# Kernel optimization log

Hardware: AMD Instinct MI355X
Metric: run time of the kernel (lower is better)

## Reference

```python
import jax, jax.numpy as jnp
import numpy as np
from jax.ops import segment_sum, segment_max

DIM = 32   # hidden dim (hardcoded in Net)
N = 10000  # nodes
E = 160000 # edges
B = 64     # graphs in batch


def setup_inputs():
    key = jax.random.key(0)
    ks = jax.random.split(key, 16)
    r = lambda k, s: jax.random.normal(k, s, dtype=jnp.float32) * 0.1
    z = lambda s: jnp.zeros(s, jnp.float32)
    return {
        "x": jax.random.normal(ks[0], (N, 1), jnp.float32),
        "edge_attr": jax.random.normal(ks[1], (E, 2), jnp.float32),
        "lin0_w": r(ks[2], (1, DIM)), "lin0_b": z((DIM,)),
        "nn_w1": r(ks[3], (2, 128)), "nn_b1": z((128,)),
        "nn_w2": r(ks[4], (128, DIM * DIM)), "nn_b2": z((DIM * DIM,)),
        "conv_root": r(ks[5], (DIM, DIM)), "conv_bias": z((DIM,)),
        "gru_w_ih": r(ks[6], (DIM, 3 * DIM)), "gru_w_hh": r(ks[7], (DIM, 3 * DIM)),
        "gru_b_ih": z((3 * DIM,)), "gru_b_hh": z((3 * DIM,)),
        "lstm_w_ih": r(ks[8], (2 * DIM, 4 * DIM)), "lstm_w_hh": r(ks[9], (DIM, 4 * DIM)),
        "lstm_b_ih": z((4 * DIM,)), "lstm_b_hh": z((4 * DIM,)),
        "lin1_w": r(ks[10], (2 * DIM, DIM)), "lin1_b": z((DIM,)),
        "lin2_w": r(ks[11], (DIM, 1)), "lin2_b": z((1,)),
        "edge_index": jax.random.randint(ks[12], (2, E), 0, N),
        "batch": jnp.sort(jax.random.randint(ks[13], (N,), 0, B)),
    }


def _forward(x, edge_attr, params, edge_index, batch):
    (lin0_w, lin0_b, nn_w1, nn_b1, nn_w2, nn_b2, conv_root, conv_bias,
     gru_w_ih, gru_w_hh, gru_b_ih, gru_b_hh,
     lstm_w_ih, lstm_w_hh, lstm_b_ih, lstm_b_hh,
     lin1_w, lin1_b, lin2_w, lin2_b) = params
    src, dst = edge_index[0], edge_index[1]
    deg = jnp.maximum(segment_sum(jnp.ones((E,), x.dtype), dst, num_segments=N), 1.0)[:, None]
    # edge-conditioned weight matrices (depend only on edge_attr -> compute once)
    ew = (jax.nn.relu(edge_attr @ nn_w1 + nn_b1) @ nn_w2 + nn_b2).reshape(E, DIM, DIM)

    out = jax.nn.relu(x @ lin0_w + lin0_b)  # (N, DIM)
    h = out                                  # GRU hidden state
    for _ in range(3):
        # NNConv: gather -> per-edge matmul -> scatter-mean, plus root weight + bias
        msg = jnp.einsum('ei,eio->eo', out[src], ew)          # (E, DIM)
        agg = segment_sum(msg, dst, num_segments=N) / deg      # (N, DIM)
        m = jax.nn.relu(agg + out @ conv_root + conv_bias)
        # single GRU step (seq_len = 1)
        gi = m @ gru_w_ih + gru_b_ih
        gh = h @ gru_w_hh + gru_b_hh
        i_r, i_z, i_n = jnp.split(gi, 3, axis=-1)
        h_r, h_z, h_n = jnp.split(gh, 3, axis=-1)
        rg = jax.nn.sigmoid(i_r + h_r)
        zg = jax.nn.sigmoid(i_z + h_z)
        ng = jnp.tanh(i_n + rg * h_n)
        h = (1.0 - zg) * ng + zg * h
        out = h

    # Set2Set pooling, 3 processing steps
    q_star = jnp.zeros((B, 2 * DIM), x.dtype)
    hh = jnp.zeros((B, DIM), x.dtype)
    cc = jnp.zeros((B, DIM), x.dtype)
    for _ in range(3):
        gates = q_star @ lstm_w_ih + lstm_b_ih + hh @ lstm_w_hh + lstm_b_hh
        ig, fg, gg, og = jnp.split(gates, 4, axis=-1)  # torch gate order i,f,g,o
        cc = jax.nn.sigmoid(fg) * cc + jax.nn.sigmoid(ig) * jnp.tanh(gg)
        hh = jax.nn.sigmoid(og) * jnp.tanh(cc)
        q = hh                                          # (B, DIM)
        e = jnp.sum(out * q[batch], axis=-1)            # (N,)
        a = jnp.exp(e - segment_max(e, batch, num_segments=B)[batch])
        a = a / segment_sum(a, batch, num_segments=B)[batch]
        rvec = segment_sum(a[:, None] * out, batch, num_segments=B)  # (B, DIM)
        q_star = jnp.concatenate([q, rvec], axis=-1)

    y = jax.nn.relu(q_star @ lin1_w + lin1_b)
    return (y @ lin2_w + lin2_b).reshape(-1)  # (B,)


def reference(x, edge_attr, lin0_w, lin0_b, nn_w1, nn_b1, nn_w2, nn_b2, conv_root, conv_bias, gru_w_ih, gru_w_hh, gru_b_ih, gru_b_hh, lstm_w_ih, lstm_w_hh, lstm_b_ih, lstm_b_hh, lin1_w, lin1_b, lin2_w, lin2_b, edge_index, batch):
    params = (lin0_w, lin0_b, nn_w1, nn_b1, nn_w2, nn_b2, conv_root, conv_bias,
              gru_w_ih, gru_w_hh, gru_b_ih, gru_b_hh,
              lstm_w_ih, lstm_w_hh, lstm_b_ih, lstm_b_hh,
              lin1_w, lin1_b, lin2_w, lin2_b)
    return _forward(x, edge_attr, params, edge_index, batch)
```

## Files before the change

kernel.cpp:

```cpp
#include <hip/hip_runtime.h>
#include <math.h>

#define NN 10000
#define NE 160000
#define NG 64
#define DIM 32
#define CAP 96

typedef __attribute__((ext_vector_type(8))) short bf16x8;
typedef __attribute__((ext_vector_type(4))) float f32x4;

__device__ __forceinline__ float sigmoidf_(float x) { return 1.f / (1.f + expf(-x)); }

__device__ __forceinline__ unsigned short f2bf(float x) {
    unsigned u = __float_as_uint(x);
    u += 0x7FFF + ((u >> 16) & 1);
    return (unsigned short)(u >> 16);
}
__device__ __forceinline__ float bf2f(unsigned short b) {
    return __uint_as_float(((unsigned)b) << 16);
}

__global__ void k_setup(const float* __restrict__ w2, unsigned short* __restrict__ w2f,
                        const float* __restrict__ x, const float* __restrict__ lw,
                        const float* __restrict__ lb, float* __restrict__ out,
                        const int* __restrict__ batch, int* __restrict__ gstart,
                        const int* __restrict__ ei, const float* __restrict__ ea,
                        int* __restrict__ cursor,
                        int* __restrict__ srt_src, float* __restrict__ srt_ea) {
    int b = blockIdx.x, t = threadIdx.x;
    if (b < 512) {
        int tid = b * 256 + t;
        int h = tid >> 10, rem = tid & 1023, i = rem >> 5, n = rem & 31;
        float v = w2[tid];
        unsigned short hi = f2bf(v);
        unsigned short lo = f2bf(v - bf2f(hi));
        int s = h >> 5, hm = h & 31, q = hm >> 3, j = hm & 7;
        int tile = n >> 4, nn = n & 15, lane = q * 16 + nn;
        int c = (i * 4 + s) * 2 + tile;
        w2f[(c * 2 + 0) * 512 + lane * 8 + j] = hi;
        w2f[(c * 2 + 1) * 512 + lane * 8 + j] = lo;
    } else if (b < 1762) {
        int idx = (b - 512) * 256 + t;
        int n = idx >> 5, d = idx & 31;
        out[idx] = fmaxf(x[n] * lw[d] + lb[d], 0.f);
    } else if (b == 1762) {
        if (t <= NG) {
            int g = t, lo = 0, hi = NN;
            while (lo < hi) { int mid = (lo + hi) >> 1; if (batch[mid] < g) lo = mid + 1; else hi = mid; }
            gstart[g] = lo;
        }
    } else {
        int e = (b - 1763) * 256 + t;
        if (e < NE) {
            int d = ei[NE + e];
            int p = atomicAdd(&cursor[d], 1);
            int pos = d * CAP + p;
            srt_src[pos] = ei[e];
            srt_ea[2 * pos]     = ea[2 * e];
            srt_ea[2 * pos + 1] = ea[2 * e + 1];
        }
    }
}

#define NS 1040
#define PS 8320
__global__ __launch_bounds__(512, 4) void k_conv_gru(
    const int* __restrict__ cursor, const int* __restrict__ srt_src,
    const float* __restrict__ srt_ea,
    const float* __restrict__ w1, const float* __restrict__ b1,
    const unsigned short* __restrict__ w2f, const float* __restrict__ b2,
    const float* __restrict__ out_old,
    float* __restrict__ Sg,
    const float* __restrict__ root, const float* __restrict__ cbias,
    const float* __restrict__ wih, const float* __restrict__ whh,
    const float* __restrict__ bih, const float* __restrict__ bhh,
    float* __restrict__ out_new)
{
    __shared__ __align__(16) unsigned short RB[2 * PS];
    int t = threadIdx.x;
    int wave = t >> 6, lane = t & 63;
    int n0 = blockIdx.x * 8;
    int n = n0 + wave;

    float Racc[64];
    #pragma unroll
    for (int i = 0; i < 64; ++i) Racc[i] = 0.f;
    float sacc = 0.f;

    float w1a0 = w1[lane],      w1c0 = w1[128 + lane],  bb0 = b1[lane];
    float w1a1 = w1[64 + lane], w1c1 = w1[192 + lane],  bb1 = b1[64 + lane];

    int rs = n * CAP;
    int re = rs + cursor[n];
    const float2* eap = (const float2*)srt_ea;

    int p = rs;
    for (; p + 1 < re; p += 2) {
        int s0 = __builtin_amdgcn_readfirstlane(srt_src[p]);
        int s1 = __builtin_amdgcn_readfirstlane(srt_src[p + 1]);
        float2 a0 = eap[p];
        float2 a1 = eap[p + 1];
        const float* o0 = out_old + s0 * DIM;
        const float* o1 = out_old + s1 * DIM;
        float r00 = fmaxf(a0.x * w1a0 + a0.y * w1c0 + bb0, 0.f);
        float r01 = fmaxf(a0.x * w1a1 + a0.y * w1c1 + bb1, 0.f);
        float r10 = fmaxf(a1.x * w1a0 + a1.y * w1c0 + bb0, 0.f);
        float r11 = fmaxf(a1.x * w1a1 + a1.y * w1c1 + bb1, 0.f);
        #pragma unroll
        for (int q = 0; q < 32; ++q) {
            float v0 = o0[q];
            Racc[q]      += r00 * v0;
            Racc[32 + q] += r01 * v0;
        }
        #pragma unroll
        for (int q = 0; q < 32; ++q) {
            float v1 = o1[q];
            Racc[q]      += r10 * v1;
            Racc[32 + q] += r11 * v1;
        }
        if (lane < DIM) sacc += o0[lane] + o1[lane];
    }
    if (p < re) {
        int s0 = __builtin_amdgcn_readfirstlane(srt_src[p]);
        float2 a0 = eap[p];
        const float* o0 = out_old + s0 * DIM;
        float r00 = fmaxf(a0.x * w1a0 + a0.y * w1c0 + bb0, 0.f);
        float r01 = fmaxf(a0.x * w1a1 + a0.y * w1c1 + bb1, 0.f);
        #pragma unroll
        for (int q = 0; q < 32; ++q) {
            float v0 = o0[q];
            Racc[q]      += r00 * v0;
            Racc[32 + q] += r01 * v0;
        }
        if (lane < DIM) sacc += o0[lane];
    }
    if (lane < DIM) Sg[n * DIM + lane] = sacc;

    int quad = lane >> 4;
    int mm = lane & 7;
    unsigned aoff = (unsigned)(mm * NS + wave * 128 + quad * 8);
    f32x4 acc0 = {0.f, 0.f, 0.f, 0.f};
    f32x4 acc1 = {0.f, 0.f, 0.f, 0.f};

    unsigned short* Hw = RB + wave * NS;
    unsigned short* Lw = RB + PS + wave * NS;

    #pragma unroll
    for (int pass = 0; pass < 4; ++pass) {
        if (pass) __syncthreads();
        #pragma unroll
        for (int li = 0; li < 8; ++li) {
            float v0 = Racc[pass * 8 + li];
            float v1 = Racc[32 + pass * 8 + li];
            unsigned short h0 = f2bf(v0);
            unsigned short l0 = f2bf(v0 - bf2f(h0));
            unsigned short h1 = f2bf(v1);
            unsigned short l1 = f2bf(v1 - bf2f(h1));
            Hw[li * 128 + lane] = h0;  Hw[li * 128 + 64 + lane] = h1;
            Lw[li * 128 + lane] = l0;  Lw[li * 128 + 64 + lane] = l1;
        }
        __syncthreads();
        int ig = pass * 8 + wave;
        #pragma unroll
        for (int s = 0; s < 4; ++s) {
            bf16x8 ah = *(const bf16x8*)(RB + aoff + s * 32);
            bf16x8 al = *(const bf16x8*)(RB + PS + aoff + s * 32);
            const unsigned short* bp = w2f + (unsigned)((ig * 4 + s) * 2048 + lane * 8);
            bf16x8 bh0 = *(const bf16x8*)(bp);
            bf16x8 bl0 = *(const bf16x8*)(bp + 512);
            bf16x8 bh1 = *(const bf16x8*)(bp + 1024);
            bf16x8 bl1 = *(const bf16x8*)(bp + 1536);
            acc0 = __builtin_amdgcn_mfma_f32_16x16x32_bf16(ah, bh0, acc0, 0, 0, 0);
            acc0 = __builtin_amdgcn_mfma_f32_16x16x32_bf16(ah, bl0, acc0, 0, 0, 0);
            acc0 = __builtin_amdgcn_mfma_f32_16x16x32_bf16(al, bh0, acc0, 0, 0, 0);
            acc1 = __builtin_amdgcn_mfma_f32_16x16x32_bf16(ah, bh1, acc1, 0, 0, 0);
            acc1 = __builtin_amdgcn_mfma_f32_16x16x32_bf16(ah, bl1, acc1, 0, 0, 0);
            acc1 = __builtin_amdgcn_mfma_f32_16x16x32_bf16(al, bh1, acc1, 0, 0, 0);
        }
    }
    __syncthreads();

    float* part = (float*)RB;
    #pragma unroll
    for (int r = 0; r < 4; ++r) {
        part[((wave * 2 + 0) * 64 + lane) * 4 + r] = acc0[r];
        part[((wave * 2 + 1) * 64 + lane) * 4 + r] = acc1[r];
    }
    __syncthreads();

    if (t < 256) {
        int nb = t >> 5, d = t & 31;
        int nn_ = n0 + nb;
        int base = t & 32;
        int tile = d >> 4, col = d & 15;
        int lidx = (nb >> 2) * 16 + col, reg = nb & 3;
        float aggv = 0.f;
        #pragma unroll
        for (int wv = 0; wv < 8; ++wv)
            aggv += part[((wv * 2 + tile) * 64 + lidx) * 4 + reg];

        float bt = 0.f;
        #pragma unroll 8
        for (int i = 0; i < DIM; ++i) bt += Sg[nn_ * DIM + i] * b2[i * DIM + d];
        int cdeg = cursor[nn_];
        float degf = (float)(cdeg > 0 ? cdeg : 1);
        aggv = (aggv + bt) / degf;

        float x = out_old[nn_ * DIM + d];
        float rootsum = 0.f;
        #pragma unroll 8
        for (int k = 0; k < DIM; ++k)
            rootsum += __shfl(x, base + k) * root[k * DIM + d];
        float m = fmaxf(aggv + rootsum + cbias[d], 0.f);

        float gir = bih[d], giz = bih[DIM + d], gin = bih[2 * DIM + d];
        float ghr = bhh[d], ghz = bhh[DIM + d], ghn = bhh[2 * DIM + d];
        #pragma unroll 4
        for (int k = 0; k < DIM; ++k) {
            float mk = __shfl(m, base + k);
            float hk = __shfl(x, base + k);
            gir += mk * wih[k * 96 + d];
            giz += mk * wih[k * 96 + DIM + d];
            gin += mk * wih[k * 96 + 2 * DIM + d];
            ghr += hk * whh[k * 96 + d];
            ghz += hk * whh[k * 96 + DIM + d];
            ghn += hk * whh[k * 96 + 2 * DIM + d];
        }
        float rg = sigmoidf_(gir + ghr);
        float zg = sigmoidf_(giz + ghz);
        float ng = tanhf(gin + rg * ghn);
        out_new[nn_ * DIM + d] = (1.f - zg) * ng + zg * x;
    }
}

__global__ __launch_bounds__(256) void k_set2set(
    const float* __restrict__ out, const int* __restrict__ gstart,
    const float* __restrict__ wih, const float* __restrict__ whh,
    const float* __restrict__ bih, const float* __restrict__ bhh,
    const float* __restrict__ l1w, const float* __restrict__ l1b,
    const float* __restrict__ l2w, const float* __restrict__ l2b,
    float* __restrict__ ebuf, float* __restrict__ y)
{
    __shared__ float swih[64 * 128];
    __shared__ float swhh[32 * 128];
    __shared__ float sq[2 * DIM];
    __shared__ float shh[DIM], scc[DIM];
    __shared__ float sgates[4 * DIM];
    __shared__ float sacc[8][DIM];
    __shared__ float sredA[4], sredB[4];

    int g = blockIdx.x, t = threadIdx.x;
    {
        const float4* wv = (const float4*)wih;   float4* sv = (float4*)swih;
        for (int i = t; i < 2048; i += 256) sv[i] = wv[i];
        const float4* wv2 = (const float4*)whh;  float4* sv2 = (float4*)swhh;
        for (int i = t; i < 1024; i += 256) sv2[i] = wv2[i];
    }
    if (t < 2 * DIM) sq[t] = 0.f;
    if (t < DIM) { shh[t] = 0.f; scc[t] = 0.f; }
    int ns = gstart[g], ne = gstart[g + 1];
    __syncthreads();

    for (int step = 0; step < 3; ++step) {
        if (t < 128) {
            float acc = bih[t] + bhh[t];
            #pragma unroll 8
            for (int k = 0; k < 2 * DIM; ++k) acc += sq[k] * swih[k * 128 + t];
            #pragma unroll 8
            for (int k = 0; k < DIM; ++k)     acc += shh[k] * swhh[k * 128 + t];
            sgates[t] = acc;
        }
        __syncthreads();
        if (t < DIM) {
            float ig = sigmoidf_(sgates[t]);
            float fg = sigmoidf_(sgates[DIM + t]);
            float gg = tanhf(sgates[2 * DIM + t]);
            float og = sigmoidf_(sgates[3 * DIM + t]);
            float c_new = fg * scc[t] + ig * gg;
            float h_new = og * tanhf(c_new);
            scc[t] = c_new;
            shh[t] = h_new;
            sq[t] = h_new;
        }
        __syncthreads();

        float lmax = -3.0e38f;
        for (int n = ns + t; n < ne; n += 256) {
            const float4* orow = (const float4*)(out + n * DIM);
            float e = 0.f;
            #pragma unroll
            for (int q = 0; q < 8; ++q) {
                float4 o4 = orow[q];
                e += o4.x * shh[4 * q] + o4.y * shh[4 * q + 1]
                   + o4.z * shh[4 * q + 2] + o4.w * shh[4 * q + 3];
            }
            ebuf[n] = e;
            lmax = fmaxf(lmax, e);
        }
        #pragma unroll
        for (int s = 1; s < 64; s <<= 1) lmax = fmaxf(lmax, __shfl_xor(lmax, s));
        if ((t & 63) == 0) sredA[t >> 6] = lmax;
        __syncthreads();
        float M = fmaxf(fmaxf(sredA[0], sredA[1]), fmaxf(sredA[2], sredA[3]));

        float lsum = 0.f;
        for (int n = ns + t; n < ne; n += 256) {
            float v = expf(ebuf[n] - M);
            ebuf[n] = v;
            lsum += v;
        }
        #pragma unroll
        for (int s = 1; s < 64; s <<= 1) lsum += __shfl_xor(lsum, s);
        if ((t & 63) == 0) sredB[t >> 6] = lsum;
        __syncthreads();
        float S = sredB[0] + sredB[1] + sredB[2] + sredB[3];
        float inv = (S > 0.f) ? 1.f / S : 0.f;

        int stp = t >> 5, d = t & 31;
        float racc = 0.f;
        for (int n = ns + stp; n < ne; n += 8)
            racc += ebuf[n] * out[n * DIM + d];
        sacc[stp][d] = racc;
        __syncthreads();
        if (t < DIM) {
            float r = 0.f;
            #pragma unroll
            for (int s = 0; s < 8; ++s) r += sacc[s][t];
            sq[DIM + t] = r * inv;
        }
        __syncthreads();
    }

    if (t < DIM) {
        float h = l1b[t];
        #pragma unroll 8
        for (int k = 0; k < 2 * DIM; ++k) h += sq[k] * l1w[k * DIM + t];
        float v = fmaxf(h, 0.f) * l2w[t];
        #pragma unroll
        for (int s = 1; s < 32; s <<= 1) v += __shfl_xor(v, s);
        if (t == 0) y[g] = v + l2b[0];
    }
}

extern "C" void kernel_launch(void* const* d_in, const int* in_sizes, int n_in,
                              void* d_out, int out_size, void* d_ws, size_t ws_size,
                              hipStream_t stream) {
    const float* x         = (const float*)d_in[0];
    const float* edge_attr = (const float*)d_in[1];
    const float* lin0_w    = (const float*)d_in[2];
    const float* lin0_b    = (const float*)d_in[3];
    const float* nn_w1     = (const float*)d_in[4];
    const float* nn_b1     = (const float*)d_in[5];
    const float* nn_w2     = (const float*)d_in[6];
    const float* nn_b2     = (const float*)d_in[7];
    const float* conv_root = (const float*)d_in[8];
    const float* conv_bias = (const float*)d_in[9];
    const float* gru_w_ih  = (const float*)d_in[10];
    const float* gru_w_hh  = (const float*)d_in[11];
    const float* gru_b_ih  = (const float*)d_in[12];
    const float* gru_b_hh  = (const float*)d_in[13];
    const float* lstm_w_ih = (const float*)d_in[14];
    const float* lstm_w_hh = (const float*)d_in[15];
    const float* lstm_b_ih = (const float*)d_in[16];
    const float* lstm_b_hh = (const float*)d_in[17];
    const float* lin1_w    = (const float*)d_in[18];
    const float* lin1_b    = (const float*)d_in[19];
    const float* lin2_w    = (const float*)d_in[20];
    const float* lin2_b    = (const float*)d_in[21];
    const int*   edge_index= (const int*)d_in[22];
    const int*   batch     = (const int*)d_in[23];
    float* yout = (float*)d_out;

    char* p = (char*)d_ws;
    auto alloc = [&](size_t bytes) { char* r = p; p += (bytes + 255) & ~(size_t)255; return r; };

    int*   cursor = (int*)  alloc(NN * sizeof(int));
    size_t zero_bytes = (size_t)(p - (char*)d_ws);
    int*   gstart    = (int*)  alloc((NG + 1) * sizeof(int));
    int*   srt_src   = (int*)  alloc((size_t)NN * CAP * sizeof(int));
    float* srt_ea    = (float*)alloc((size_t)NN * CAP * 2 * sizeof(float));
    float* outA      = (float*)alloc(NN * DIM * sizeof(float));
    float* outB      = (float*)alloc(NN * DIM * sizeof(float));
    float* Sg        = (float*)alloc(NN * DIM * sizeof(float));
    unsigned short* w2f = (unsigned short*)alloc(262144 * sizeof(unsigned short));
    float* ebuf      = (float*)alloc(NN * sizeof(float));
    (void)ws_size; (void)n_in; (void)in_sizes; (void)out_size;

    hipMemsetAsync(d_ws, 0, zero_bytes, stream);

    k_setup<<<2388, 256, 0, stream>>>(nn_w2, w2f, x, lin0_w, lin0_b, outA, batch, gstart,
                                      edge_index, edge_attr, cursor, srt_src, srt_ea);

    const float* cur = outA;
    float* nxt = outB;
    for (int it = 0; it < 3; ++it) {
        k_conv_gru<<<1250, 512, 0, stream>>>(cursor, srt_src, srt_ea,
                                             nn_w1, nn_b1, w2f, nn_b2,
                                             cur, Sg,
                                             conv_root, conv_bias,
                                             gru_w_ih, gru_w_hh, gru_b_ih, gru_b_hh,
                                             nxt);
        const float* tmp = nxt; nxt = (float*)cur; cur = tmp;
    }
    const float* outF = cur;

    k_set2set<<<NG, 256, 0, stream>>>(outF, gstart,
                                      lstm_w_ih, lstm_w_hh, lstm_b_ih, lstm_b_hh,
                                      lin1_w, lin1_b, lin2_w, lin2_b, ebuf, yout);
}
```

Baseline: 327.8 us.

## Sort nodes by degree for balanced blocks and preload edge lists per wave

Adds a single-block k_perm kernel that buckets nodes by in-degree (descending) into a permutation, so each 8-wave conv block handles nodes of similar degree and waves inside a block wait less on each other. The conv kernel also loads up to 64 edge sources and attributes per wave in one coalesced load and broadcasts them with readlane, replacing per-edge scalar loads. The per-node neighbor sum moves from a global Sg buffer into shared memory, using all 64 lanes before a final shuffle reduction. It adds an extra serial kernel launch and indirect node indexing, which scatters the output writes.

```diff
diff --git a/kernel.cpp b/kernel.cpp
--- a/kernel.cpp
+++ b/kernel.cpp
@@ -6,6 +6,7 @@
 #define NG 64
 #define DIM 32
 #define CAP 96
+#define NBIN (CAP + 1)
 
 typedef __attribute__((ext_vector_type(8))) short bf16x8;
 typedef __attribute__((ext_vector_type(4))) float f32x4;
@@ -19,6 +20,9 @@
 }
 __device__ __forceinline__ float bf2f(unsigned short b) {
     return __uint_as_float(((unsigned)b) << 16);
+}
+__device__ __forceinline__ float rlanef(float v, int i) {
+    return __uint_as_float((unsigned)__builtin_amdgcn_readlane((int)__float_as_uint(v), i));
 }
 
 __global__ void k_setup(const float* __restrict__ w2, unsigned short* __restrict__ w2f,
@@ -63,25 +67,71 @@
     }
 }
 
+__global__ __launch_bounds__(1024) void k_perm(const int* __restrict__ cursor,
+                                               int* __restrict__ perm) {
+    __shared__ int hist[NBIN * 16];
+    __shared__ int binsum[NBIN];
+    __shared__ int base[NBIN];
+    int t = threadIdx.x;
+    for (int i = t; i < NBIN * 16; i += 1024) hist[i] = 0;
+    __syncthreads();
+    int sub = t & 15;
+    for (int n = t; n < NN; n += 1024) {
+        int d = cursor[n]; d = d > CAP ? CAP : d;
+        atomicAdd(&hist[d * 16 + sub], 1);
+    }
+    __syncthreads();
+    if (t < NBIN) {
+        int s = 0;
+        #pragma unroll
+        for (int k = 0; k < 16; ++k) s += hist[t * 16 + k];
+        binsum[t] = s;
+    }
+    __syncthreads();
+    if (t == 0) {
+        int acc = 0;
+        for (int d = CAP; d >= 0; --d) { base[d] = acc; acc += binsum[d]; }
+    }
+    __syncthreads();
+    if (t < NBIN) {
+        int acc = base[t];
+        #pragma unroll
+        for (int k = 0; k < 16; ++k) {
+            int c = hist[t * 16 + k];
+            hist[t * 16 + k] = acc;
+            acc += c;
+        }
+    }
+    __syncthreads();
+    for (int n = t; n < NN; n += 1024) {
+        int d = cursor[n]; d = d > CAP ? CAP : d;
+        int pos = atomicAdd(&hist[d * 16 + sub], 1);
+        perm[pos] = n;
+    }
+}
+
 #define NS 1040
 #define PS 8320
 __global__ __launch_bounds__(512, 4) void k_conv_gru(
+    const int* __restrict__ perm,
     const int* __restrict__ cursor, const int* __restrict__ srt_src,
     const float* __restrict__ srt_ea,
     const float* __restrict__ w1, const float* __restrict__ b1,
     const unsigned short* __restrict__ w2f, const float* __restrict__ b2,
     const float* __restrict__ out_old,
-    float* __restrict__ Sg,
     const float* __restrict__ root, const float* __restrict__ cbias,
     const float* __restrict__ wih, const float* __restrict__ whh,
     const float* __restrict__ bih, const float* __restrict__ bhh,
     float* __restrict__ out_new)
 {
     __shared__ __align__(16) unsigned short RB[2 * PS];
+    __shared__ float sSg[8][DIM];
+    __shared__ int sNode[8];
     int t = threadIdx.x;
     int wave = t >> 6, lane = t & 63;
     int n0 = blockIdx.x * 8;
-    int n = n0 + wave;
+    int n = perm[n0 + wave];
+    if (lane == 0) sNode[wave] = n;
 
     float Racc[64];
     #pragma unroll
@@ -91,22 +141,30 @@
     float w1a0 = w1[lane],      w1c0 = w1[128 + lane],  bb0 = b1[lane];
     float w1a1 = w1[64 + lane], w1c1 = w1[192 + lane],  bb1 = b1[64 + lane];
 
+    int deg = cursor[n];
     int rs = n * CAP;
-    int re = rs + cursor[n];
     const float2* eap = (const float2*)srt_ea;
 
-    int p = rs;
-    for (; p + 1 < re; p += 2) {
-        int s0 = __builtin_amdgcn_readfirstlane(srt_src[p]);
-        int s1 = __builtin_amdgcn_readfirstlane(srt_src[p + 1]);
-        float2 a0 = eap[p];
-        float2 a1 = eap[p + 1];
+    int msrc = 0; float mex = 0.f, mey = 0.f;
+    if (lane < deg) {
+        msrc = srt_src[rs + lane];
+        float2 a = eap[rs + lane];
+        mex = a.x; mey = a.y;
+    }
+
+    int dmain = deg < 64 ? deg : 64;
+    int i = 0;
+    for (; i + 1 < dmain; i += 2) {
+        int s0 = __builtin_amdgcn_readlane(msrc, i);
+        int s1 = __builtin_amdgcn_readlane(msrc, i + 1);
+        float a0x = rlanef(mex, i),     a0y = rlanef(mey, i);
+        float a1x = rlanef(mex, i + 1), a1y = rlanef(mey, i + 1);
         const float* o0 = out_old + s0 * DIM;
         const float* o1 = out_old + s1 * DIM;
-        float r00 = fmaxf(a0.x * w1a0 + a0.y * w1c0 + bb0, 0.f);
-        float r01 = fmaxf(a0.x * w1a1 + a0.y * w1c1 + bb1, 0.f);
-        float r10 = fmaxf(a1.x * w1a0 + a1.y * w1c0 + bb0, 0.f);
-        float r11 = fmaxf(a1.x * w1a1 + a1.y * w1c1 + bb1, 0.f);
+        float r00 = fmaxf(a0x * w1a0 + a0y * w1c0 + bb0, 0.f);
+        float r01 = fmaxf(a0x * w1a1 + a0y * w1c1 + bb1, 0.f);
+        float r10 = fmaxf(a1x * w1a0 + a1y * w1c0 + bb0, 0.f);
+        float r11 = fmaxf(a1x * w1a1 + a1y * w1c1 + bb1, 0.f);
         #pragma unroll
         for (int q = 0; q < 32; ++q) {
             float v0 = o0[q];
@@ -119,9 +177,24 @@
             Racc[q]      += r10 * v1;
             Racc[32 + q] += r11 * v1;
         }
-        if (lane < DIM) sacc += o0[lane] + o1[lane];
-    }
-    if (p < re) {
+        const float* oc = (lane < 32) ? (o0 + lane) : (o1 + lane - 32);
+        sacc += *oc;
+    }
+    if (i < dmain) {
+        int s0 = __builtin_amdgcn_readlane(msrc, i);
+        float a0x = rlanef(mex, i), a0y = rlanef(mey, i);
+        const float* o0 = out_old + s0 * DIM;
+        float r00 = fmaxf(a0x * w1a0 + a0y * w1c0 + bb0, 0.f);
+        float r01 = fmaxf(a0x * w1a1 + a0y * w1c1 + bb1, 0.f);
+        #pragma unroll
+        for (int q = 0; q < 32; ++q) {
+            float v0 = o0[q];
+            Racc[q]      += r00 * v0;
+            Racc[32 + q] += r01 * v0;
+        }
+        if (lane < 32) sacc += o0[lane];
+    }
+    for (int p = rs + 64; p < rs + deg; ++p) {
         int s0 = __builtin_amdgcn_readfirstlane(srt_src[p]);
         float2 a0 = eap[p];
         const float* o0 = out_old + s0 * DIM;
@@ -133,9 +206,10 @@
             Racc[q]      += r00 * v0;
             Racc[32 + q] += r01 * v0;
         }
-        if (lane < DIM) sacc += o0[lane];
-    }
-    if (lane < DIM) Sg[n * DIM + lane] = sacc;
+        if (lane < 32) sacc += o0[lane];
+    }
+    sacc += __shfl_xor(sacc, 32);
+    if (lane < DIM) sSg[wave][lane] = sacc;
 
     int quad = lane >> 4;
     int mm = lane & 7;
@@ -191,7 +265,7 @@
 
     if (t < 256) {
         int nb = t >> 5, d = t & 31;
-        int nn_ = n0 + nb;
+        int nn_ = sNode[nb];
         int base = t & 32;
         int tile = d >> 4, col = d & 15;
         int lidx = (nb >> 2) * 16 + col, reg = nb & 3;
@@ -202,7 +276,7 @@
 
         float bt = 0.f;
         #pragma unroll 8
-        for (int i = 0; i < DIM; ++i) bt += Sg[nn_ * DIM + i] * b2[i * DIM + d];
+        for (int i2 = 0; i2 < DIM; ++i2) bt += sSg[nb][i2] * b2[i2 * DIM + d];
         int cdeg = cursor[nn_];
         float degf = (float)(cdeg > 0 ? cdeg : 1);
         aggv = (aggv + bt) / degf;
@@ -382,7 +456,7 @@
     float* srt_ea    = (float*)alloc((size_t)NN * CAP * 2 * sizeof(float));
     float* outA      = (float*)alloc(NN * DIM * sizeof(float));
     float* outB      = (float*)alloc(NN * DIM * sizeof(float));
-    float* Sg        = (float*)alloc(NN * DIM * sizeof(float));
+    int*   perm      = (int*)  alloc(NN * sizeof(int));
     unsigned short* w2f = (unsigned short*)alloc(262144 * sizeof(unsigned short));
     float* ebuf      = (float*)alloc(NN * sizeof(float));
     (void)ws_size; (void)n_in; (void)in_sizes; (void)out_size;
@@ -391,13 +465,14 @@
 
     k_setup<<<2388, 256, 0, stream>>>(nn_w2, w2f, x, lin0_w, lin0_b, outA, batch, gstart,
                                       edge_index, edge_attr, cursor, srt_src, srt_ea);
+    k_perm<<<1, 1024, 0, stream>>>(cursor, perm);
 
     const float* cur = outA;
     float* nxt = outB;
     for (int it = 0; it < 3; ++it) {
-        k_conv_gru<<<1250, 512, 0, stream>>>(cursor, srt_src, srt_ea,
+        k_conv_gru<<<1250, 512, 0, stream>>>(perm, cursor, srt_src, srt_ea,
                                              nn_w1, nn_b1, w2f, nn_b2,
-                                             cur, Sg,
+                                             cur,
                                              conv_root, conv_bias,
                                              gru_w_ih, gru_w_hh, gru_b_ih, gru_b_hh,
                                              nxt);
```

Result: faster. 314.9 us (-3.9%).
